# Performance work log

Hardware: AMD Instinct MI355X
Metric: run time of the kernel (lower is better)

The kernel has to match this reference:

```python
import jax, jax.numpy as jnp
import numpy as np

N = 50000
E = 800000
IN_DIM = 128
HID = 64
HEADS = 4
NUM_CLASSES = 40
NEG_SLOPE = 0.2
BN_EPS = 1e-5
SM_EPS = 1e-16


def setup_inputs() -> dict:
    key = jax.random.key(0)
    ks = jax.random.split(key, 12)
    d1 = HID * HEADS
    s_in = 1.0 / np.sqrt(IN_DIM)
    s_d1 = 1.0 / np.sqrt(d1)
    return {
        "x": jax.random.normal(ks[0], (N, IN_DIM), dtype=jnp.float32),
        "edge_index": jax.random.randint(ks[1], (2, E), 0, N, dtype=jnp.int32),
        # layer 1 (heads=4, concat)
        "Wl1": jax.random.normal(ks[2], (IN_DIM, d1), dtype=jnp.float32) * s_in,
        "Wr1": jax.random.normal(ks[3], (IN_DIM, d1), dtype=jnp.float32) * s_in,
        "att1": jax.random.normal(ks[4], (HEADS, HID), dtype=jnp.float32) * (1.0 / np.sqrt(HID)),
        "b1": jnp.zeros((d1,), dtype=jnp.float32),
        "gamma1": jnp.ones((d1,), dtype=jnp.float32),
        "beta1": jnp.zeros((d1,), dtype=jnp.float32),
        # layer 2 (heads=1, mean)
        "Wl2": jax.random.normal(ks[5], (d1, NUM_CLASSES), dtype=jnp.float32) * s_d1,
        "Wr2": jax.random.normal(ks[6], (d1, NUM_CLASSES), dtype=jnp.float32) * s_d1,
        "att2": jax.random.normal(ks[7], (1, NUM_CLASSES), dtype=jnp.float32) * (1.0 / np.sqrt(NUM_CLASSES)),
        "b2": jnp.zeros((NUM_CLASSES,), dtype=jnp.float32),
    }


def _gatv2_conv(x, Wl, Wr, att, b, src, dst, heads, out_ch, concat):
    n = x.shape[0]
    xl = (x @ Wl).reshape(n, heads, out_ch)   # source transform
    xr = (x @ Wr).reshape(n, heads, out_ch)   # target transform
    # per-edge attention logits (GATv2): a^T LeakyReLU(xl_j + xr_i)
    s = xl[src] + xr[dst]                                    # [E, H, C]
    e = jnp.einsum('ehc,hc->eh', jax.nn.leaky_relu(s, NEG_SLOPE), att)  # [E, H]
    # segment softmax over incoming edges of each dst node
    m = jax.ops.segment_max(e, dst, num_segments=n)          # [N, H]
    a = jnp.exp(e - m[dst])
    denom = jax.ops.segment_sum(a, dst, num_segments=n)
    alpha = a / (denom[dst] + SM_EPS)                        # [E, H]
    # aggregate messages alpha * xl_j
    out = jax.ops.segment_sum(alpha[..., None] * xl[src], dst, num_segments=n)  # [N, H, C]
    out = out.reshape(n, heads * out_ch) if concat else out.mean(axis=1)
    return out + b


def _batchnorm(h, gamma, beta):
    mu = h.mean(axis=0)
    var = h.var(axis=0)
    return gamma * (h - mu) * jax.lax.rsqrt(var + BN_EPS) + beta


def reference(x, edge_index, Wl1, Wr1, att1, b1, gamma1, beta1, Wl2, Wr2, att2, b2):
    n = x.shape[0]
    # add self-loops (PyG GATv2Conv default add_self_loops=True)
    loop = jnp.arange(n, dtype=edge_index.dtype)
    src = jnp.concatenate([edge_index[0], loop])
    dst = jnp.concatenate([edge_index[1], loop])
    h = _gatv2_conv(x, Wl1, Wr1, att1, b1, src, dst, HEADS, HID, True)
    h = jax.nn.elu(_batchnorm(h, gamma1, beta1))
    # eval mode: dropout is identity
    return _gatv2_conv(h, Wl2, Wr2, att2, b2, src, dst, 1, NUM_CLASSES, False)
```

## Files before the change

kernel.cpp:

```cpp
#include <hip/hip_runtime.h>
#include <math.h>

#define N_NODES 50000
#define N_EDGES 800000
#define ET (N_EDGES + N_NODES)
#define IN_DIM 128
#define HID 64
#define HEADS 4
#define D1 256
#define NCLS 40
#define NEG_SLOPE 0.2f
#define BN_EPS 1e-5f
#define SM_EPS 1e-16f
#define NB 196
#define DEGB 3321
#define XB 6250

typedef unsigned short ushort_t;
typedef __attribute__((ext_vector_type(8))) short short8;
typedef __attribute__((ext_vector_type(16))) float f32x16;

__device__ __forceinline__ float eluf(float x) { return x > 0.f ? x : expm1f(x); }
__device__ __forceinline__ float lrelu(float x) { return x >= 0.f ? x : NEG_SLOPE * x; }
__device__ __forceinline__ unsigned short f2bf(float f) {
    unsigned int u = __float_as_uint(f);
    u += 0x7fffu + ((u >> 16) & 1u);
    return (unsigned short)(u >> 16);
}
__device__ __forceinline__ float bf2f(ushort_t u) {
    return __uint_as_float(((unsigned int)u) << 16);
}

__global__ __launch_bounds__(256) void k_prep(
    const int* __restrict__ ei, int* __restrict__ deg,
    const float* __restrict__ x, ushort_t* __restrict__ xb,
    const float* __restrict__ Wl1, const float* __restrict__ Wr1,
    ushort_t* __restrict__ BT1,
    const float* __restrict__ Wl2, const float* __restrict__ Wr2,
    ushort_t* __restrict__ BT2)
{
    const int b = blockIdx.x, t = threadIdx.x;
    if (b < DEGB) {
        int e = b * 256 + t;
        if (e < ET) {
            int dst = (e < N_EDGES) ? ei[N_EDGES + e] : (e - N_EDGES);
            atomicAdd(&deg[dst], 1);
        }
    } else if (b < DEGB + XB) {
        int i = (b - DEGB) * 256 + t;
        float4 v = ((const float4*)x)[i];
        ushort4 o;
        o.x = f2bf(v.x); o.y = f2bf(v.y); o.z = f2bf(v.z); o.w = f2bf(v.w);
        ((ushort4*)xb)[i] = o;
    } else if (b < DEGB + XB + 256) {
        int n = (b - DEGB - XB) * 2 + (t >> 7);
        int k = t & 127;
        float v = (n < 256) ? Wl1[k * 256 + n] : Wr1[k * 256 + (n - 256)];
        BT1[n * 128 + k] = f2bf(v);
    } else {
        int n = b - DEGB - XB - 256;
        int k = t;
        float v = 0.f;
        if (n < 40)      v = Wl2[k * 40 + n];
        else if (n < 80) v = Wr2[k * 40 + (n - 40)];
        BT2[n * 256 + k] = f2bf(v);
    }
}

__global__ __launch_bounds__(256) void k_scan1(const int* __restrict__ deg,
                                               int* __restrict__ row_st,
                                               int* __restrict__ bsum) {
    __shared__ int wsum[4], woff[4];
    const int t = threadIdx.x, w = t >> 6, lane = t & 63;
    const int idx = blockIdx.x * 256 + t;
    int v = (idx < N_NODES) ? deg[idx] : 0;
    int s = v;
    #pragma unroll
    for (int off = 1; off < 64; off <<= 1) {
        int y = __shfl_up(s, off, 64);
        if (lane >= off) s += y;
    }
    if (lane == 63) wsum[w] = s;
    __syncthreads();
    if (t == 0) {
        int run = 0;
        #pragma unroll
        for (int i2 = 0; i2 < 4; i2++) { woff[i2] = run; run += wsum[i2]; }
        bsum[blockIdx.x] = run;
    }
    __syncthreads();
    if (idx < N_NODES) row_st[idx] = woff[w] + (s - v);
}

__global__ __launch_bounds__(256) void k_scan3(int* __restrict__ row_st,
                                               int* __restrict__ cursor,
                                               const int* __restrict__ bsum) {
    __shared__ int wred[4];
    const int t = threadIdx.x, w = t >> 6, lane = t & 63;
    int part = 0;
    for (int j = t; j < blockIdx.x; j += 256) part += bsum[j];
    #pragma unroll
    for (int off = 32; off; off >>= 1) part += __shfl_xor(part, off, 64);
    if (lane == 0) wred[w] = part;
    __syncthreads();
    const int pre = wred[0] + wred[1] + wred[2] + wred[3];
    const int idx = blockIdx.x * 256 + t;
    if (idx < N_NODES) {
        int r = row_st[idx] + pre;
        row_st[idx] = r;
        cursor[idx] = r;
    }
    if (idx == 0) row_st[N_NODES] = ET;
}

__global__ void k_scatter(const int* __restrict__ ei, int* __restrict__ cursor,
                          int* __restrict__ csr_src) {
    int e = blockIdx.x * blockDim.x + threadIdx.x;
    if (e >= ET) return;
    int src, dst;
    if (e < N_EDGES) { src = ei[e]; dst = ei[N_EDGES + e]; }
    else             { src = dst = e - N_EDGES; }
    int pos = atomicAdd(&cursor[dst], 1);
    csr_src[pos] = src;
}

#define MBM 128
#define MBN 128
#define MBK 64
template<typename OT>
__global__ __launch_bounds__(256) void k_mgemm(
    const ushort_t* __restrict__ A, const ushort_t* __restrict__ BT,
    OT* __restrict__ C, int M, int K, int N, int ldc)
{
    __shared__ __align__(16) ushort_t Al[MBM * MBK];
    __shared__ __align__(16) ushort_t Bl[MBN * MBK];
    const int t = threadIdx.x;
    const int w = t >> 6, L = t & 63;
    const int i0 = blockIdx.x * MBM;
    const int j0 = blockIdx.y * MBN;
    const int wm = (w >> 1) * 64, wn = (w & 1) * 64;
    const int l31 = L & 31, half = L >> 5;

    int sm[4], sca[4];
    #pragma unroll
    for (int r = 0; r < 4; r++) {
        int s = (r * 4 + w) * 64 + L;
        int m = s >> 3;
        sm[r] = m;
        sca[r] = (s & 7) ^ (m & 7);
    }

    f32x16 acc[2][2];
    #pragma unroll
    for (int a = 0; a < 2; a++)
        #pragma unroll
        for (int b = 0; b < 2; b++)
            #pragma unroll
            for (int r = 0; r < 16; r++) acc[a][b][r] = 0.f;

    for (int kt = 0; kt < K; kt += MBK) {
        short8 sa[4], sb[4];
        #pragma unroll
        for (int r = 0; r < 4; r++) {
            int row = i0 + sm[r]; if (row >= M) row = M - 1;
            sa[r] = *(const short8*)&A[(size_t)row * K + kt + sca[r] * 8];
            sb[r] = *(const short8*)&BT[(size_t)(j0 + sm[r]) * K + kt + sca[r] * 8];
        }
        __syncthreads();
        #pragma unroll
        for (int r = 0; r < 4; r++) {
            int s = (r * 4 + w) * 64 + L;
            *(short8*)&Al[s * 8] = sa[r];
            *(short8*)&Bl[s * 8] = sb[r];
        }
        __syncthreads();
        #pragma unroll
        for (int ks = 0; ks < 4; ks++) {
            short8 af[2], bfr[2];
            #pragma unroll
            for (int mt = 0; mt < 2; mt++) {
                int m = wm + mt * 32 + l31;
                int c = (ks * 2 + half) ^ (m & 7);
                af[mt] = *(const short8*)&Al[(m * 8 + c) * 8];
            }
            #pragma unroll
            for (int nt = 0; nt < 2; nt++) {
                int n = wn + nt * 32 + l31;
                int c = (ks * 2 + half) ^ (n & 7);
                bfr[nt] = *(const short8*)&Bl[(n * 8 + c) * 8];
            }
            #pragma unroll
            for (int mt = 0; mt < 2; mt++)
                #pragma unroll
                for (int nt = 0; nt < 2; nt++)
                    acc[mt][nt] = __builtin_amdgcn_mfma_f32_32x32x16_bf16(
                        af[mt], bfr[nt], acc[mt][nt], 0, 0, 0);
        }
    }
    #pragma unroll
    for (int mt = 0; mt < 2; mt++)
        #pragma unroll
        for (int nt = 0; nt < 2; nt++) {
            int col = j0 + wn + nt * 32 + l31;
            int rbase = i0 + wm + mt * 32 + 4 * half;
            if (col < N) {
                #pragma unroll
                for (int r = 0; r < 16; r++) {
                    int row = rbase + (r & 3) + 8 * (r >> 2);
                    if (row < M) {
                        if constexpr (sizeof(OT) == 2)
                            C[(size_t)row * ldc + col] = (OT)f2bf(acc[mt][nt][r]);
                        else
                            C[(size_t)row * ldc + col] = acc[mt][nt][r];
                    }
                }
            }
        }
}

__global__ __launch_bounds__(256) void k_mgemm_bn(
    const float* __restrict__ A, const ushort_t* __restrict__ BT,
    ushort_t* __restrict__ C, int M, int K, int N, int ldc,
    const float* __restrict__ bn_sum, const float* __restrict__ bn_sumsq,
    const float* __restrict__ gamma, const float* __restrict__ beta)
{
    __shared__ __align__(16) ushort_t Al[MBM * MBK];
    __shared__ __align__(16) ushort_t Bl[MBN * MBK];
    __shared__ float gsh[256], bsh[256];
    const int t = threadIdx.x;
    const int w = t >> 6, L = t & 63;
    const int i0 = blockIdx.x * MBM;
    const int j0 = blockIdx.y * MBN;
    const int wm = (w >> 1) * 64, wn = (w & 1) * 64;
    const int l31 = L & 31, half = L >> 5;
    {
        float mean = bn_sum[t] * (1.f / N_NODES);
        float var = bn_sumsq[t] * (1.f / N_NODES) - mean * mean;
        float g = gamma[t] * rsqrtf(var + BN_EPS);
        gsh[t] = g;
        bsh[t] = beta[t] - g * mean;
    }
    __syncthreads();

    int sm[4], sca[4];
    #pragma unroll
    for (int r = 0; r < 4; r++) {
        int s = (r * 4 + w) * 64 + L;
        int m = s >> 3;
        sm[r] = m;
        sca[r] = (s & 7) ^ (m & 7);
    }

    f32x16 acc[2][2];
    #pragma unroll
    for (int a = 0; a < 2; a++)
        #pragma unroll
        for (int b = 0; b < 2; b++)
            #pragma unroll
            for (int r = 0; r < 16; r++) acc[a][b][r] = 0.f;

    for (int kt = 0; kt < K; kt += MBK) {
        short8 sa[4], sb[4];
        #pragma unroll
        for (int r = 0; r < 4; r++) {
            int row = i0 + sm[r]; if (row >= M) row = M - 1;
            int kb = kt + sca[r] * 8;
            float4 v0 = *(const float4*)&A[(size_t)row * K + kb];
            float4 v1 = *(const float4*)&A[(size_t)row * K + kb + 4];
            float4 g0 = *(const float4*)&gsh[kb];
            float4 g1 = *(const float4*)&gsh[kb + 4];
            float4 b0 = *(const float4*)&bsh[kb];
            float4 b1v = *(const float4*)&bsh[kb + 4];
            short8 o;
            o[0] = (short)f2bf(eluf(g0.x * v0.x + b0.x));
            o[1] = (short)f2bf(eluf(g0.y * v0.y + b0.y));
            o[2] = (short)f2bf(eluf(g0.z * v0.z + b0.z));
            o[3] = (short)f2bf(eluf(g0.w * v0.w + b0.w));
            o[4] = (short)f2bf(eluf(g1.x * v1.x + b1v.x));
            o[5] = (short)f2bf(eluf(g1.y * v1.y + b1v.y));
            o[6] = (short)f2bf(eluf(g1.z * v1.z + b1v.z));
            o[7] = (short)f2bf(eluf(g1.w * v1.w + b1v.w));
            sa[r] = o;
            sb[r] = *(const short8*)&BT[(size_t)(j0 + sm[r]) * K + kb];
        }
        __syncthreads();
        #pragma unroll
        for (int r = 0; r < 4; r++) {
            int s = (r * 4 + w) * 64 + L;
            *(short8*)&Al[s * 8] = sa[r];
            *(short8*)&Bl[s * 8] = sb[r];
        }
        __syncthreads();
        #pragma unroll
        for (int ks = 0; ks < 4; ks++) {
            short8 af[2], bfr[2];
            #pragma unroll
            for (int mt = 0; mt < 2; mt++) {
                int m = wm + mt * 32 + l31;
                int c = (ks * 2 + half) ^ (m & 7);
                af[mt] = *(const short8*)&Al[(m * 8 + c) * 8];
            }
            #pragma unroll
            for (int nt = 0; nt < 2; nt++) {
                int n = wn + nt * 32 + l31;
                int c = (ks * 2 + half) ^ (n & 7);
                bfr[nt] = *(const short8*)&Bl[(n * 8 + c) * 8];
            }
            #pragma unroll
            for (int mt = 0; mt < 2; mt++)
                #pragma unroll
                for (int nt = 0; nt < 2; nt++)
                    acc[mt][nt] = __builtin_amdgcn_mfma_f32_32x32x16_bf16(
                        af[mt], bfr[nt], acc[mt][nt], 0, 0, 0);
        }
    }
    #pragma unroll
    for (int mt = 0; mt < 2; mt++)
        #pragma unroll
        for (int nt = 0; nt < 2; nt++) {
            int col = j0 + wn + nt * 32 + l31;
            int rbase = i0 + wm + mt * 32 + 4 * half;
            if (col < N) {
                #pragma unroll
                for (int r = 0; r < 16; r++) {
                    int row = rbase + (r & 3) + 8 * (r >> 2);
                    if (row < M)
                        C[(size_t)row * ldc + col] = f2bf(acc[mt][nt][r]);
                }
            }
        }
}

#define CH1 16
#define XLS 260
__global__ __launch_bounds__(256) void k_node1(
    const ushort_t* __restrict__ xlr, const int* __restrict__ row_start,
    const int* __restrict__ csr_src, const float* __restrict__ att1,
    const float* __restrict__ b1, float* __restrict__ h1)
{
    __shared__ __align__(16) float xl_sh[CH1 * XLS];
    __shared__ __align__(16) float p_sh[HEADS][CH1];
    const int i = blockIdx.x;
    const int t = threadIdx.x;
    const int h = t >> 6, lane = t & 63;
    const int qe = lane >> 2, qq = lane & 3;
    const int half = lane >> 5, l31 = lane & 31;
    const int s0 = row_start[i], s1 = row_start[i + 1];
    const int e0 = h * 2 + half, e1 = 8 + h * 2 + half;

    float xr_t[16], at_t[16];
    {
        const ushort_t* xrp = &xlr[(size_t)i * 512 + 256 + h * 64 + qq * 16];
        const float* atp = &att1[h * 64 + qq * 16];
        #pragma unroll
        for (int k = 0; k < 16; k += 4) {
            ushort4 u = *(const ushort4*)&xrp[k];
            float4 b = *(const float4*)&atp[k];
            xr_t[k + 0] = bf2f(u.x); xr_t[k + 1] = bf2f(u.y);
            xr_t[k + 2] = bf2f(u.z); xr_t[k + 3] = bf2f(u.w);
            at_t[k + 0] = b.x; at_t[k + 1] = b.y; at_t[k + 2] = b.z; at_t[k + 3] = b.w;
        }
    }
    const float bvv = b1[t];

    float acc = 0.f, l_run = 0.f;

    int base = s0;
    const int nfull = (s1 - s0) >> 4;
    int src0 = csr_src[min(s0 + e0, s1 - 1)];
    int src1 = csr_src[min(s0 + e1, s1 - 1)];
    for (int f = 0; f < nfull; f++, base += CH1) {
        __syncthreads();
        {
            const ushort_t* gp0 = &xlr[(size_t)src0 * 512];
            ushort4 a0 = *(const ushort4*)&gp0[4 * l31];
            ushort4 a1 = *(const ushort4*)&gp0[128 + 4 * l31];
            const ushort_t* gp1 = &xlr[(size_t)src1 * 512];
            ushort4 c0 = *(const ushort4*)&gp1[4 * l31];
            ushort4 c1 = *(const ushort4*)&gp1[128 + 4 * l31];
            *(float4*)&xl_sh[e0 * XLS + 4 * l31] =
                make_float4(bf2f(a0.x), bf2f(a0.y), bf2f(a0.z), bf2f(a0.w));
            *(float4*)&xl_sh[e0 * XLS + 128 + 4 * l31] =
                make_float4(bf2f(a1.x), bf2f(a1.y), bf2f(a1.z), bf2f(a1.w));
            *(float4*)&xl_sh[e1 * XLS + 4 * l31] =
                make_float4(bf2f(c0.x), bf2f(c0.y), bf2f(c0.z), bf2f(c0.w));
            *(float4*)&xl_sh[e1 * XLS + 128 + 4 * l31] =
                make_float4(bf2f(c1.x), bf2f(c1.y), bf2f(c1.z), bf2f(c1.w));
        }
        __syncthreads();
        {
            int nb = base + CH1;
            src0 = csr_src[min(nb + e0, s1 - 1)];
            src1 = csr_src[min(nb + e1, s1 - 1)];
        }
        float dot = 0.f;
        {
            const float* xp = &xl_sh[qe * XLS + h * 64 + qq * 16];
            #pragma unroll
            for (int k = 0; k < 16; k += 4) {
                float4 v = *(const float4*)&xp[k];
                dot += lrelu(v.x + xr_t[k + 0]) * at_t[k + 0];
                dot += lrelu(v.y + xr_t[k + 1]) * at_t[k + 1];
                dot += lrelu(v.z + xr_t[k + 2]) * at_t[k + 2];
                dot += lrelu(v.w + xr_t[k + 3]) * at_t[k + 3];
            }
        }
        dot += __shfl_xor(dot, 1, 64);
        dot += __shfl_xor(dot, 2, 64);
        if (qq == 0) p_sh[h][qe] = __expf(dot);
        float4 P0 = *(const float4*)&p_sh[h][0];
        float4 P1 = *(const float4*)&p_sh[h][4];
        float4 P2 = *(const float4*)&p_sh[h][8];
        float4 P3 = *(const float4*)&p_sh[h][12];
        float p[16] = {P0.x, P0.y, P0.z, P0.w, P1.x, P1.y, P1.z, P1.w,
                       P2.x, P2.y, P2.z, P2.w, P3.x, P3.y, P3.z, P3.w};
        float lsum = 0.f;
        #pragma unroll
        for (int e = 0; e < 16; e++) lsum += p[e];
        l_run += lsum;
        #pragma unroll
        for (int e = 0; e < 16; e++)
            acc += p[e] * xl_sh[e * XLS + t];
    }
    const int rem = s1 - base;
    if (rem > 0) {
        __syncthreads();
        if (e0 < rem) {
            const ushort_t* gp = &xlr[(size_t)src0 * 512];
            ushort4 u0 = *(const ushort4*)&gp[4 * l31];
            ushort4 u1 = *(const ushort4*)&gp[128 + 4 * l31];
            *(float4*)&xl_sh[e0 * XLS + 4 * l31] =
                make_float4(bf2f(u0.x), bf2f(u0.y), bf2f(u0.z), bf2f(u0.w));
            *(float4*)&xl_sh[e0 * XLS + 128 + 4 * l31] =
                make_float4(bf2f(u1.x), bf2f(u1.y), bf2f(u1.z), bf2f(u1.w));
        }
        if (e1 < rem) {
            const ushort_t* gp = &xlr[(size_t)src1 * 512];
            ushort4 u0 = *(const ushort4*)&gp[4 * l31];
            ushort4 u1 = *(const ushort4*)&gp[128 + 4 * l31];
            *(float4*)&xl_sh[e1 * XLS + 4 * l31] =
                make_float4(bf2f(u0.x), bf2f(u0.y), bf2f(u0.z), bf2f(u0.w));
            *(float4*)&xl_sh[e1 * XLS + 128 + 4 * l31] =
                make_float4(bf2f(u1.x), bf2f(u1.y), bf2f(u1.z), bf2f(u1.w));
        }
        __syncthreads();
        float dot = 0.f;
        {
            const float* xp = &xl_sh[qe * XLS + h * 64 + qq * 16];
            #pragma unroll
            for (int k = 0; k < 16; k += 4) {
                float4 v = *(const float4*)&xp[k];
                dot += lrelu(v.x + xr_t[k + 0]) * at_t[k + 0];
                dot += lrelu(v.y + xr_t[k + 1]) * at_t[k + 1];
                dot += lrelu(v.z + xr_t[k + 2]) * at_t[k + 2];
                dot += lrelu(v.w + xr_t[k + 3]) * at_t[k + 3];
            }
        }
        dot += __shfl_xor(dot, 1, 64);
        dot += __shfl_xor(dot, 2, 64);
        if (qq == 0) p_sh[h][qe] = (qe < rem) ? __expf(dot) : 0.f;
        for (int e = 0; e < rem; e++) {
            float pe = p_sh[h][e];
            l_run += pe;
            acc += pe * xl_sh[e * XLS + t];
        }
    }
    h1[(size_t)i * 256 + t] = acc / (l_run + SM_EPS) + bvv;
}

__global__ void k_bnstats(const float* __restrict__ h1, float* __restrict__ bn_sum,
                          float* __restrict__ bn_sumsq) {
    const int t = threadIdx.x;
    const int rows_per = (N_NODES + gridDim.x - 1) / gridDim.x;
    const int r0 = blockIdx.x * rows_per;
    const int r1 = min(N_NODES, r0 + rows_per);
    float s = 0.f, s2 = 0.f;
    for (int r = r0; r < r1; r++) {
        float v = h1[(size_t)r * 256 + t];
        s += v; s2 += v * v;
    }
    atomicAdd(&bn_sum[t], s);
    atomicAdd(&bn_sumsq[t], s2);
}

#define C2S 44
__global__ __launch_bounds__(256) void k_node2(
    const ushort_t* __restrict__ xlr2, const int* __restrict__ row_start,
    const int* __restrict__ csr_src, const float* __restrict__ att2,
    const float* __restrict__ b2, float* __restrict__ out)
{
    __shared__ __align__(16) float xl_sh[4][16 * C2S];
    __shared__ __align__(16) float p_sh[4][16];
    __shared__ int src_sh[4][16];
    const int wv = threadIdx.x >> 6, L = threadIdx.x & 63;
    const int i = blockIdx.x * 4 + wv;
    const int qe = L >> 2, qq = L & 3;
    const bool node_ok = (i < N_NODES);
    int s0 = 0, s1 = 0;
    if (node_ok) { s0 = row_start[i]; s1 = row_start[i + 1]; }
    float at_t[10], xr_t[10];
    #pragma unroll
    for (int r = 0; r < 10; r++) at_t[r] = att2[qq + 4 * r];
    if (node_ok) {
        const ushort_t* xrp = &xlr2[(size_t)i * 80 + 40];
        #pragma unroll
        for (int r = 0; r < 10; r++) xr_t[r] = bf2f(xrp[qq + 4 * r]);
    }

    float accv = 0.f, l_run = 0.f;
    const int cagg = (L < NCLS) ? L : 0;
    const int e16 = L & 15, k16 = L >> 4;

    if (node_ok) {
        int base = s0;
        const int nfull = (s1 - s0) >> 4;
        for (int f = 0; f < nfull; f++, base += 16) {
            if (L < 16) src_sh[wv][L] = csr_src[base + L];
            {
                short8 u = *(const short8*)&xlr2[(size_t)src_sh[wv][e16] * 80 + k16 * 8];
                float4 f0 = make_float4(bf2f((ushort_t)u[0]), bf2f((ushort_t)u[1]),
                                        bf2f((ushort_t)u[2]), bf2f((ushort_t)u[3]));
                float4 f1 = make_float4(bf2f((ushort_t)u[4]), bf2f((ushort_t)u[5]),
                                        bf2f((ushort_t)u[6]), bf2f((ushort_t)u[7]));
                *(float4*)&xl_sh[wv][e16 * C2S + k16 * 8] = f0;
                *(float4*)&xl_sh[wv][e16 * C2S + k16 * 8 + 4] = f1;
                if (L < 16) {
                    short8 u2 = *(const short8*)&xlr2[(size_t)src_sh[wv][L] * 80 + 32];
                    float4 g0 = make_float4(bf2f((ushort_t)u2[0]), bf2f((ushort_t)u2[1]),
                                            bf2f((ushort_t)u2[2]), bf2f((ushort_t)u2[3]));
                    float4 g1 = make_float4(bf2f((ushort_t)u2[4]), bf2f((ushort_t)u2[5]),
                                            bf2f((ushort_t)u2[6]), bf2f((ushort_t)u2[7]));
                    *(float4*)&xl_sh[wv][L * C2S + 32] = g0;
                    *(float4*)&xl_sh[wv][L * C2S + 36] = g1;
                }
            }
            float dot = 0.f;
            #pragma unroll
            for (int r = 0; r < 10; r++) {
                float v = xl_sh[wv][qe * C2S + qq + 4 * r];
                dot += lrelu(v + xr_t[r]) * at_t[r];
            }
            dot += __shfl_xor(dot, 1, 64);
            dot += __shfl_xor(dot, 2, 64);
            if (qq == 0) p_sh[wv][qe] = __expf(dot);
            float4 P0 = *(const float4*)&p_sh[wv][0];
            float4 P1 = *(const float4*)&p_sh[wv][4];
            float4 P2 = *(const float4*)&p_sh[wv][8];
            float4 P3 = *(const float4*)&p_sh[wv][12];
            float p[16] = {P0.x, P0.y, P0.z, P0.w, P1.x, P1.y, P1.z, P1.w,
                           P2.x, P2.y, P2.z, P2.w, P3.x, P3.y, P3.z, P3.w};
            float lsum = 0.f;
            #pragma unroll
            for (int e = 0; e < 16; e++) lsum += p[e];
            l_run += lsum;
            #pragma unroll
            for (int e = 0; e < 16; e++)
                accv += p[e] * xl_sh[wv][e * C2S + cagg];
        }
        const int rem = s1 - base;
        if (rem > 0) {
            if (L < rem) src_sh[wv][L] = csr_src[base + L];
            if (e16 < rem) {
                short8 u = *(const short8*)&xlr2[(size_t)src_sh[wv][e16] * 80 + k16 * 8];
                float4 f0 = make_float4(bf2f((ushort_t)u[0]), bf2f((ushort_t)u[1]),
                                        bf2f((ushort_t)u[2]), bf2f((ushort_t)u[3]));
                float4 f1 = make_float4(bf2f((ushort_t)u[4]), bf2f((ushort_t)u[5]),
                                        bf2f((ushort_t)u[6]), bf2f((ushort_t)u[7]));
                *(float4*)&xl_sh[wv][e16 * C2S + k16 * 8] = f0;
                *(float4*)&xl_sh[wv][e16 * C2S + k16 * 8 + 4] = f1;
            }
            if (L < rem) {
                short8 u2 = *(const short8*)&xlr2[(size_t)src_sh[wv][L] * 80 + 32];
                float4 g0 = make_float4(bf2f((ushort_t)u2[0]), bf2f((ushort_t)u2[1]),
                                        bf2f((ushort_t)u2[2]), bf2f((ushort_t)u2[3]));
                float4 g1 = make_float4(bf2f((ushort_t)u2[4]), bf2f((ushort_t)u2[5]),
                                        bf2f((ushort_t)u2[6]), bf2f((ushort_t)u2[7]));
                *(float4*)&xl_sh[wv][L * C2S + 32] = g0;
                *(float4*)&xl_sh[wv][L * C2S + 36] = g1;
            }
            float dot = 0.f;
            #pragma unroll
            for (int r = 0; r < 10; r++) {
                float v = xl_sh[wv][qe * C2S + qq + 4 * r];
                dot += lrelu(v + xr_t[r]) * at_t[r];
            }
            dot += __shfl_xor(dot, 1, 64);
            dot += __shfl_xor(dot, 2, 64);
            if (qq == 0) p_sh[wv][qe] = (qe < rem) ? __expf(dot) : 0.f;
            for (int e = 0; e < rem; e++) {
                float pe = p_sh[wv][e];
                l_run += pe;
                accv += pe * xl_sh[wv][e * C2S + cagg];
            }
        }
    }
    if (node_ok && L < NCLS)
        out[(size_t)i * 40 + L] = accv / (l_run + SM_EPS) + b2[L];
}

static inline size_t align_up(size_t v, size_t a) { return (v + a - 1) & ~(a - 1); }

extern "C" void kernel_launch(void* const* d_in, const int* in_sizes, int n_in,
                              void* d_out, int out_size, void* d_ws, size_t ws_size,
                              hipStream_t stream)
{
    const float* x     = (const float*)d_in[0];
    const int*   ei    = (const int*)d_in[1];
    const float* Wl1   = (const float*)d_in[2];
    const float* Wr1   = (const float*)d_in[3];
    const float* att1  = (const float*)d_in[4];
    const float* b1    = (const float*)d_in[5];
    const float* gamma1= (const float*)d_in[6];
    const float* beta1 = (const float*)d_in[7];
    const float* Wl2   = (const float*)d_in[8];
    const float* Wr2   = (const float*)d_in[9];
    const float* att2  = (const float*)d_in[10];
    const float* b2    = (const float*)d_in[11];
    float* out = (float*)d_out;

    char* ws = (char*)d_ws;
    size_t off = 0;
    ushort_t* xlr1b = (ushort_t*)(ws + off); off += (size_t)N_NODES * 512 * 2;
    float*    h1    = (float*)   (ws + off); off += (size_t)N_NODES * 256 * 4;
    int*   csr_src = (int*)  (ws + off); off += align_up((size_t)ET * 4, 256);
    int*   row_st  = (int*)  (ws + off); off += align_up((size_t)(N_NODES + 1) * 4, 256);
    int*   cursor  = (int*)  (ws + off); off += align_up((size_t)N_NODES * 4, 256);
    int*   bsum    = (int*)  (ws + off); off += align_up((size_t)NB * 4, 256);
    size_t zoff = off;
    int*   deg     = (int*)  (ws + off); off += align_up((size_t)N_NODES * 4, 256);
    float* bn_sum  = (float*)(ws + off); off += 256 * 4;
    float* bn_sumsq= (float*)(ws + off); off += 256 * 4;
    size_t zlen = off - zoff;
    ushort_t* BT1  = (ushort_t*)(ws + off); off += align_up((size_t)512 * 128 * 2, 256);
    ushort_t* BT2  = (ushort_t*)(ws + off); off += align_up((size_t)128 * 256 * 2, 256);
    ushort_t* xlr2b = xlr1b;
    ushort_t* xb    = (ushort_t*)h1;

    hipMemsetAsync(ws + zoff, 0, zlen, stream);

    k_prep<<<DEGB + XB + 256 + 128, 256, 0, stream>>>(
        ei, deg, x, xb, Wl1, Wr1, BT1, Wl2, Wr2, BT2);
    k_scan1<<<NB, 256, 0, stream>>>(deg, row_st, bsum);
    k_scan3<<<NB, 256, 0, stream>>>(row_st, cursor, bsum);
    k_scatter<<<DEGB, 256, 0, stream>>>(ei, cursor, csr_src);

    dim3 g1((N_NODES + MBM - 1) / MBM, 512 / MBN);
    k_mgemm<ushort_t><<<g1, 256, 0, stream>>>(xb, BT1, xlr1b, N_NODES, IN_DIM, 512, 512);
    k_node1<<<N_NODES, 256, 0, stream>>>(xlr1b, row_st, csr_src, att1, b1, h1);

    k_bnstats<<<1000, 256, 0, stream>>>(h1, bn_sum, bn_sumsq);

    dim3 g2((N_NODES + MBM - 1) / MBM, 1);
    k_mgemm_bn<<<g2, 256, 0, stream>>>(h1, BT2, xlr2b, N_NODES, D1, 80, 80,
                                       bn_sum, bn_sumsq, gamma1, beta1);
    k_node2<<<(N_NODES + 3) / 4, 256, 0, stream>>>(xlr2b, row_st, csr_src, att2, b2, out);
}
```

Measured before the change: 428.7 us.

## Fuse BN statistics into node1 aggregation, store h1 as bf16, algebraic leaky-relu

Removes the separate BN statistics kernel. k_node1 now accumulates per-channel sum and sum-of-squares with atomics spread over 64 slices, and k_mgemm_bn reduces those slices when it starts. The h1 intermediate is stored as bf16 instead of fp32, which halves its write and read traffic. The leaky-relu-times-attention dot products are rewritten as 0.6*a*y + 0.4*a*|y| fused multiply-adds. In exchange this adds 512 atomics per node and loses some precision in h1 before batch norm.

After: 443.8 us. 3.5% more time.

```diff
diff --git a/kernel.cpp b/kernel.cpp
--- a/kernel.cpp
+++ b/kernel.cpp
@@ -15,6 +15,7 @@
 #define NB 196
 #define DEGB 3321
 #define XB 6250
+#define BNSL 64
 
 typedef unsigned short ushort_t;
 typedef __attribute__((ext_vector_type(8))) short short8;
@@ -219,9 +220,9 @@
 }
 
 __global__ __launch_bounds__(256) void k_mgemm_bn(
-    const float* __restrict__ A, const ushort_t* __restrict__ BT,
+    const ushort_t* __restrict__ A, const ushort_t* __restrict__ BT,
     ushort_t* __restrict__ C, int M, int K, int N, int ldc,
-    const float* __restrict__ bn_sum, const float* __restrict__ bn_sumsq,
+    const float* __restrict__ bn_ps, const float* __restrict__ bn_sq,
     const float* __restrict__ gamma, const float* __restrict__ beta)
 {
     __shared__ __align__(16) ushort_t Al[MBM * MBK];
@@ -234,8 +235,14 @@
     const int wm = (w >> 1) * 64, wn = (w & 1) * 64;
     const int l31 = L & 31, half = L >> 5;
     {
-        float mean = bn_sum[t] * (1.f / N_NODES);
-        float var = bn_sumsq[t] * (1.f / N_NODES) - mean * mean;
+        float s = 0.f, s2 = 0.f;
+        #pragma unroll 8
+        for (int j = 0; j < BNSL; j++) {
+            s += bn_ps[j * 256 + t];
+            s2 += bn_sq[j * 256 + t];
+        }
+        float mean = s * (1.f / N_NODES);
+        float var = s2 * (1.f / N_NODES) - mean * mean;
         float g = gamma[t] * rsqrtf(var + BN_EPS);
         gsh[t] = g;
         bsh[t] = beta[t] - g * mean;
@@ -265,21 +272,20 @@
         for (int r = 0; r < 4; r++) {
             int row = i0 + sm[r]; if (row >= M) row = M - 1;
             int kb = kt + sca[r] * 8;
-            float4 v0 = *(const float4*)&A[(size_t)row * K + kb];
-            float4 v1 = *(const float4*)&A[(size_t)row * K + kb + 4];
+            short8 u = *(const short8*)&A[(size_t)row * K + kb];
             float4 g0 = *(const float4*)&gsh[kb];
             float4 g1 = *(const float4*)&gsh[kb + 4];
             float4 b0 = *(const float4*)&bsh[kb];
             float4 b1v = *(const float4*)&bsh[kb + 4];
             short8 o;
-            o[0] = (short)f2bf(eluf(g0.x * v0.x + b0.x));
-            o[1] = (short)f2bf(eluf(g0.y * v0.y + b0.y));
-            o[2] = (short)f2bf(eluf(g0.z * v0.z + b0.z));
-            o[3] = (short)f2bf(eluf(g0.w * v0.w + b0.w));
-            o[4] = (short)f2bf(eluf(g1.x * v1.x + b1v.x));
-            o[5] = (short)f2bf(eluf(g1.y * v1.y + b1v.y));
-            o[6] = (short)f2bf(eluf(g1.z * v1.z + b1v.z));
-            o[7] = (short)f2bf(eluf(g1.w * v1.w + b1v.w));
+            o[0] = (short)f2bf(eluf(g0.x * bf2f((ushort_t)u[0]) + b0.x));
+            o[1] = (short)f2bf(eluf(g0.y * bf2f((ushort_t)u[1]) + b0.y));
+            o[2] = (short)f2bf(eluf(g0.z * bf2f((ushort_t)u[2]) + b0.z));
+            o[3] = (short)f2bf(eluf(g0.w * bf2f((ushort_t)u[3]) + b0.w));
+            o[4] = (short)f2bf(eluf(g1.x * bf2f((ushort_t)u[4]) + b1v.x));
+            o[5] = (short)f2bf(eluf(g1.y * bf2f((ushort_t)u[5]) + b1v.y));
+            o[6] = (short)f2bf(eluf(g1.z * bf2f((ushort_t)u[6]) + b1v.z));
+            o[7] = (short)f2bf(eluf(g1.w * bf2f((ushort_t)u[7]) + b1v.w));
             sa[r] = o;
             sb[r] = *(const short8*)&BT[(size_t)(j0 + sm[r]) * K + kb];
         }
@@ -336,7 +342,8 @@
 __global__ __launch_bounds__(256) void k_node1(
     const ushort_t* __restrict__ xlr, const int* __restrict__ row_start,
     const int* __restrict__ csr_src, const float* __restrict__ att1,
-    const float* __restrict__ b1, float* __restrict__ h1)
+    const float* __restrict__ b1, ushort_t* __restrict__ h1b,
+    float* __restrict__ bn_ps, float* __restrict__ bn_sq)
 {
     __shared__ __align__(16) float xl_sh[CH1 * XLS];
     __shared__ __align__(16) float p_sh[HEADS][CH1];
@@ -348,7 +355,7 @@
     const int s0 = row_start[i], s1 = row_start[i + 1];
     const int e0 = h * 2 + half, e1 = 8 + h * 2 + half;
 
-    float xr_t[16], at_t[16];
+    float xr_t[16], at6[16], at4[16];
     {
         const ushort_t* xrp = &xlr[(size_t)i * 512 + 256 + h * 64 + qq * 16];
         const float* atp = &att1[h * 64 + qq * 16];
@@ -358,7 +365,10 @@
             float4 b = *(const float4*)&atp[k];
             xr_t[k + 0] = bf2f(u.x); xr_t[k + 1] = bf2f(u.y);
             xr_t[k + 2] = bf2f(u.z); xr_t[k + 3] = bf2f(u.w);
-            at_t[k + 0] = b.x; at_t[k + 1] = b.y; at_t[k + 2] = b.z; at_t[k + 3] = b.w;
+            at6[k + 0] = 0.6f * b.x; at6[k + 1] = 0.6f * b.y;
+            at6[k + 2] = 0.6f * b.z; at6[k + 3] = 0.6f * b.w;
+            at4[k + 0] = 0.4f * b.x; at4[k + 1] = 0.4f * b.y;
+            at4[k + 2] = 0.4f * b.z; at4[k + 3] = 0.4f * b.w;
         }
     }
     const float bvv = b1[t];
@@ -399,10 +409,12 @@
             #pragma unroll
             for (int k = 0; k < 16; k += 4) {
                 float4 v = *(const float4*)&xp[k];
-                dot += lrelu(v.x + xr_t[k + 0]) * at_t[k + 0];
-                dot += lrelu(v.y + xr_t[k + 1]) * at_t[k + 1];
-                dot += lrelu(v.z + xr_t[k + 2]) * at_t[k + 2];
-                dot += lrelu(v.w + xr_t[k + 3]) * at_t[k + 3];
+                float y0 = v.x + xr_t[k + 0], y1 = v.y + xr_t[k + 1];
+                float y2 = v.z + xr_t[k + 2], y3 = v.w + xr_t[k + 3];
+                dot = __builtin_fmaf(at6[k + 0], y0, __builtin_fmaf(at4[k + 0], __builtin_fabsf(y0), dot));
+                dot = __builtin_fmaf(at6[k + 1], y1, __builtin_fmaf(at4[k + 1], __builtin_fabsf(y1), dot));
+                dot = __builtin_fmaf(at6[k + 2], y2, __builtin_fmaf(at4[k + 2], __builtin_fabsf(y2), dot));
+                dot = __builtin_fmaf(at6[k + 3], y3, __builtin_fmaf(at4[k + 3], __builtin_fabsf(y3), dot));
             }
         }
         dot += __shfl_xor(dot, 1, 64);
@@ -450,10 +462,12 @@
             #pragma unroll
             for (int k = 0; k < 16; k += 4) {
                 float4 v = *(const float4*)&xp[k];
-                dot += lrelu(v.x + xr_t[k + 0]) * at_t[k + 0];
-                dot += lrelu(v.y + xr_t[k + 1]) * at_t[k + 1];
-                dot += lrelu(v.z + xr_t[k + 2]) * at_t[k + 2];
-                dot += lrelu(v.w + xr_t[k + 3]) * at_t[k + 3];
+                float y0 = v.x + xr_t[k + 0], y1 = v.y + xr_t[k + 1];
+                float y2 = v.z + xr_t[k + 2], y3 = v.w + xr_t[k + 3];
+                dot = __builtin_fmaf(at6[k + 0], y0, __builtin_fmaf(at4[k + 0], __builtin_fabsf(y0), dot));
+                dot = __builtin_fmaf(at6[k + 1], y1, __builtin_fmaf(at4[k + 1], __builtin_fabsf(y1), dot));
+                dot = __builtin_fmaf(at6[k + 2], y2, __builtin_fmaf(at4[k + 2], __builtin_fabsf(y2), dot));
+                dot = __builtin_fmaf(at6[k + 3], y3, __builtin_fmaf(at4[k + 3], __builtin_fabsf(y3), dot));
             }
         }
         dot += __shfl_xor(dot, 1, 64);
@@ -465,22 +479,11 @@
             acc += pe * xl_sh[e * XLS + t];
         }
     }
-    h1[(size_t)i * 256 + t] = acc / (l_run + SM_EPS) + bvv;
-}
-
-__global__ void k_bnstats(const float* __restrict__ h1, float* __restrict__ bn_sum,
-                          float* __restrict__ bn_sumsq) {
-    const int t = threadIdx.x;
-    const int rows_per = (N_NODES + gridDim.x - 1) / gridDim.x;
-    const int r0 = blockIdx.x * rows_per;
-    const int r1 = min(N_NODES, r0 + rows_per);
-    float s = 0.f, s2 = 0.f;
-    for (int r = r0; r < r1; r++) {
-        float v = h1[(size_t)r * 256 + t];
-        s += v; s2 += v * v;
-    }
-    atomicAdd(&bn_sum[t], s);
-    atomicAdd(&bn_sumsq[t], s2);
+    const float val = acc / (l_run + SM_EPS) + bvv;
+    h1b[(size_t)i * 256 + t] = f2bf(val);
+    const int sl = (i & (BNSL - 1)) * 256 + t;
+    atomicAdd(&bn_ps[sl], val);
+    atomicAdd(&bn_sq[sl], val * val);
 }
 
 #define C2S 44
@@ -498,9 +501,12 @@
     const bool node_ok = (i < N_NODES);
     int s0 = 0, s1 = 0;
     if (node_ok) { s0 = row_start[i]; s1 = row_start[i + 1]; }
-    float at_t[10], xr_t[10];
-    #pragma unroll
-    for (int r = 0; r < 10; r++) at_t[r] = att2[qq + 4 * r];
+    float at6[10], at4[10], xr_t[10];
+    #pragma unroll
+    for (int r = 0; r < 10; r++) {
+        float a = att2[qq + 4 * r];
+        at6[r] = 0.6f * a; at4[r] = 0.4f * a;
+    }
     if (node_ok) {
         const ushort_t* xrp = &xlr2[(size_t)i * 80 + 40];
         #pragma unroll
@@ -537,8 +543,8 @@
             float dot = 0.f;
             #pragma unroll
             for (int r = 0; r < 10; r++) {
-                float v = xl_sh[wv][qe * C2S + qq + 4 * r];
-                dot += lrelu(v + xr_t[r]) * at_t[r];
+                float y = xl_sh[wv][qe * C2S + qq + 4 * r] + xr_t[r];
+                dot = __builtin_fmaf(at6[r], y, __builtin_fmaf(at4[r], __builtin_fabsf(y), dot));
             }
             dot += __shfl_xor(dot, 1, 64);
             dot += __shfl_xor(dot, 2, 64);
@@ -581,8 +587,8 @@
             float dot = 0.f;
             #pragma unroll
             for (int r = 0; r < 10; r++) {
-                float v = xl_sh[wv][qe * C2S + qq + 4 * r];
-                dot += lrelu(v + xr_t[r]) * at_t[r];
+                float y = xl_sh[wv][qe * C2S + qq + 4 * r] + xr_t[r];
+                dot = __builtin_fmaf(at6[r], y, __builtin_fmaf(at4[r], __builtin_fabsf(y), dot));
             }
             dot += __shfl_xor(dot, 1, 64);
             dot += __shfl_xor(dot, 2, 64);
@@ -621,20 +627,20 @@
     char* ws = (char*)d_ws;
     size_t off = 0;
     ushort_t* xlr1b = (ushort_t*)(ws + off); off += (size_t)N_NODES * 512 * 2;
-    float*    h1    = (float*)   (ws + off); off += (size_t)N_NODES * 256 * 4;
+    ushort_t* h1b   = (ushort_t*)(ws + off); off += (size_t)N_NODES * 256 * 2;
+    ushort_t* xb    = (ushort_t*)(ws + off); off += (size_t)N_NODES * IN_DIM * 2;
     int*   csr_src = (int*)  (ws + off); off += align_up((size_t)ET * 4, 256);
     int*   row_st  = (int*)  (ws + off); off += align_up((size_t)(N_NODES + 1) * 4, 256);
     int*   cursor  = (int*)  (ws + off); off += align_up((size_t)N_NODES * 4, 256);
     int*   bsum    = (int*)  (ws + off); off += align_up((size_t)NB * 4, 256);
     size_t zoff = off;
     int*   deg     = (int*)  (ws + off); off += align_up((size_t)N_NODES * 4, 256);
-    float* bn_sum  = (float*)(ws + off); off += 256 * 4;
-    float* bn_sumsq= (float*)(ws + off); off += 256 * 4;
+    float* bn_ps   = (float*)(ws + off); off += (size_t)BNSL * 256 * 4;
+    float* bn_sq   = (float*)(ws + off); off += (size_t)BNSL * 256 * 4;
     size_t zlen = off - zoff;
     ushort_t* BT1  = (ushort_t*)(ws + off); off += align_up((size_t)512 * 128 * 2, 256);
     ushort_t* BT2  = (ushort_t*)(ws + off); off += align_up((size_t)128 * 256 * 2, 256);
     ushort_t* xlr2b = xlr1b;
-    ushort_t* xb    = (ushort_t*)h1;
 
     hipMemsetAsync(ws + zoff, 0, zlen, stream);
 
@@ -646,12 +652,11 @@
 
     dim3 g1((N_NODES + MBM - 1) / MBM, 512 / MBN);
     k_mgemm<ushort_t><<<g1, 256, 0, stream>>>(xb, BT1, xlr1b, N_NODES, IN_DIM, 512, 512);
-    k_node1<<<N_NODES, 256, 0, stream>>>(xlr1b, row_st, csr_src, att1, b1, h1);
-
-    k_bnstats<<<1000, 256, 0, stream>>>(h1, bn_sum, bn_sumsq);
+    k_node1<<<N_NODES, 256, 0, stream>>>(xlr1b, row_st, csr_src, att1, b1, h1b,
+                                         bn_ps, bn_sq);
 
     dim3 g2((N_NODES + MBM - 1) / MBM, 1);
-    k_mgemm_bn<<<g2, 256, 0, stream>>>(h1, BT2, xlr2b, N_NODES, D1, 80, 80,
-                                       bn_sum, bn_sumsq, gamma1, beta1);
+    k_mgemm_bn<<<g2, 256, 0, stream>>>(h1b, BT2, xlr2b, N_NODES, D1, 80, 80,
+                                       bn_ps, bn_sq, gamma1, beta1);
     k_node2<<<(N_NODES + 3) / 4, 256, 0, stream>>>(xlr2b, row_st, csr_src, att2, b2, out);
 }
```
